# Performance work log

Measured on AMD Instinct MI355X. Metric: run time of the kernel, lower is better.

The kernel has to match this reference:

```python
import jax, jax.numpy as jnp
import numpy as np

B, S, D = 8, 1024, 512


def setup_inputs() -> dict:
    key = jax.random.key(0)
    k1, k2, k3, k4, k5, k6, k7 = jax.random.split(key, 7)
    inp = jax.random.normal(k1, (B, S, D), dtype=jnp.float32)
    aspect = jax.random.normal(k2, (B, S, D), dtype=jnp.float32)
    # lengths in [S//2, S], with max exactly S (the module requires max(len)==S)
    inp_len = jax.random.randint(k3, (B,), S // 2, S + 1).astype(jnp.float32)
    inp_len = inp_len.at[0].set(float(S))
    lim = float(np.sqrt(6.0 / (D + D)))  # xavier_uniform bound
    w1 = jax.random.uniform(k4, (D, D), jnp.float32, -lim, lim)
    b1 = jax.random.uniform(k5, (D,), jnp.float32, -lim, lim)
    w2 = jax.random.uniform(k6, (D, D), jnp.float32, -lim, lim)
    b2 = jax.random.uniform(k7, (D,), jnp.float32, -lim, lim)
    return {"inp": inp, "inp_len": inp_len, "aspect": aspect,
            "w1": w1, "b1": b1, "w2": w2, "b2": b2}


def reference(inp, inp_len, aspect, w1, b1, w2, b2):
    # inp, aspect: [B,S,D]; inp_len: [B] float lengths with max == S
    Bv, Sv, Dv = inp.shape
    scale = jnp.sqrt(inp_len)[:, None, None]                      # [B,1,1]
    att = jnp.einsum('bsd,btd->bst', aspect, inp) / scale          # [B,S,S]
    # mask over the query (row) dimension, as in the original expand
    mask = (jnp.arange(Sv)[None, :] < inp_len.astype(jnp.int32)[:, None]).astype(inp.dtype)  # [B,S]
    exp = att * mask[:, :, None]
    att_n = exp / (jnp.sum(exp, axis=-1, keepdims=True) + 1e-4)    # linear (non-exp) normalize
    weighted = jnp.einsum('bst,btd->bsd', att_n, inp)              # [B,S,D]
    ffn_inp = weighted + (inp + aspect) * mask[:, :, None]
    # FFN: two square linears with relu, plus inner residual
    o1 = jax.nn.relu(jnp.einsum('bsd,ed->bse', ffn_inp, w1) + b1)
    o2 = jax.nn.relu(jnp.einsum('bsd,ed->bse', o1, w2) + b2)
    ffn_out = o2 + ffn_inp
    final = ffn_inp + ffn_out
    return final / jnp.linalg.norm(final, axis=2, keepdims=True)
```

## Files before the change

kernel.cpp:

```cpp
#include <hip/hip_runtime.h>

#define Bq 8
#define Sq 1024
#define Dq 512

typedef __attribute__((ext_vector_type(8))) short bf16x8;
typedef __attribute__((ext_vector_type(4))) float f32x4;

__device__ __forceinline__ unsigned short f2bf(float f) {
  unsigned int u = __float_as_uint(f);
  return (unsigned short)((u + 0x7fffu + ((u >> 16) & 1u)) >> 16);
}

__device__ __forceinline__ void load_lds16(const unsigned short* g, unsigned short* l) {
  __builtin_amdgcn_global_load_lds(
      (const __attribute__((address_space(1))) unsigned int*)g,
      (__attribute__((address_space(3))) unsigned int*)l, 16, 0, 0);
}


__global__ __launch_bounds__(256) void prep_t(
    const float* __restrict__ inp,
    unsigned short* __restrict__ inpT, float* __restrict__ partial) {
  __shared__ unsigned short tile[64][66];
  __shared__ float csum[16][64];
  int idx = blockIdx.x;
  int tid = threadIdx.x;
  int b = idx & 7, tt = (idx >> 3) & 15, dd = idx >> 7;
  int r = tid >> 4, c4 = (tid & 15) * 4;
  const float* src = inp + ((size_t)b * Sq + tt * 64) * Dq + dd * 64;
  float cp0 = 0.f, cp1 = 0.f, cp2 = 0.f, cp3 = 0.f;
#pragma unroll
  for (int p = 0; p < 4; ++p) {
    float4 v = *(const float4*)(src + (size_t)(r + p * 16) * Dq + c4);
    ushort4 o; o.x = f2bf(v.x); o.y = f2bf(v.y); o.z = f2bf(v.z); o.w = f2bf(v.w);
    *(ushort4*)&tile[r + p * 16][c4] = o;
    cp0 += v.x; cp1 += v.y; cp2 += v.z; cp3 += v.w;
  }
  csum[r][c4] = cp0; csum[r][c4 + 1] = cp1; csum[r][c4 + 2] = cp2; csum[r][c4 + 3] = cp3;
  __syncthreads();
  unsigned short* dst = inpT + (size_t)b * Dq * Sq + (size_t)dd * 64 * Sq + tt * 64;
#pragma unroll
  for (int p = 0; p < 4; ++p) {
    int d = (tid >> 4) + p * 16;
    int tq = (tid & 15) * 4;
    ushort4 o;
    o.x = tile[tq][d]; o.y = tile[tq + 1][d]; o.z = tile[tq + 2][d]; o.w = tile[tq + 3][d];
    *(ushort4*)(dst + (size_t)d * Sq + tq) = o;
  }
  if (tid < 64) {
    float s = 0.f;
#pragma unroll
    for (int rr = 0; rr < 16; ++rr) s += csum[rr][tid];
    partial[((size_t)b * 16 + tt) * Dq + dd * 64 + tid] = s;
  }
}

__global__ __launch_bounds__(512, 2) void gram_fac(
    const unsigned short* __restrict__ inpT, const float* __restrict__ partial,
    const float* __restrict__ aspect, const float* __restrict__ lenv,
    const float* __restrict__ w1, const float* __restrict__ w2,
    unsigned short* __restrict__ Gm, float* __restrict__ fac,
    unsigned short* __restrict__ asp_bf,
    unsigned short* __restrict__ w1b, unsigned short* __restrict__ w2b) {
  __shared__ unsigned short sA[2][64 * 64];
  __shared__ unsigned short sB[2][128 * 64];
  int idx = blockIdx.x;
  int tid = threadIdx.x;
  int lane = tid & 63, wave = tid >> 6;

  if (idx >= 672) {
    int blk = idx - 672;
    const float* src = (blk < 128) ? w1 : w2;
    unsigned short* dst = (blk < 128) ? w1b : w2b;
    int li = ((blk & 127) * 512 + tid) * 4;
    int n = li >> 9, k = li & 511;
    float4 v = *(const float4*)(src + li);
    ushort4 o; o.x = f2bf(v.x); o.y = f2bf(v.y); o.z = f2bf(v.z); o.w = f2bf(v.w);
    int x = ((k >> 3) & 3) ^ ((n >> 1) & 3);
    int off = (k >> 5) * 16384 + n * 32 + x * 8 + (k & 7);
    *(ushort4*)(dst + off) = o;
    return;
  }
  if (idx >= 416) {
    int blk = idx - 416;
    const float* s = aspect + (size_t)blk * 16384 + tid * 4;
    unsigned short* d = asp_bf + (size_t)blk * 16384 + tid * 4;
#pragma unroll
    for (int j = 0; j < 8; ++j) {
      float4 v = *(const float4*)(s + j * 2048);
      ushort4 o; o.x = f2bf(v.x); o.y = f2bf(v.y); o.z = f2bf(v.z); o.w = f2bf(v.w);
      *(ushort4*)(d + j * 2048) = o;
    }
    return;
  }
  if (idx >= 160) {
    float* cs = (float*)sA;
    int fblk = idx - 160;
    int b = fblk >> 5;
    int s0 = (fblk & 31) * 32;
    {
      int d = tid;
      float s = 0.f;
      const float* p = partial + (size_t)b * 16 * Dq + d;
#pragma unroll
      for (int t = 0; t < 16; ++t) s += p[t * Dq];
      cs[d] = s;
    }
    __syncthreads();
    int g = lane >> 4, lr = lane & 15;
    int row = s0 + wave * 4 + g;
    const float* a = aspect + ((size_t)b * Sq + row) * Dq + lr * 32;
    float sum = 0.f;
#pragma unroll
    for (int j = 0; j < 8; ++j) {
      float4 v = *(const float4*)(a + j * 4);
      const float* c = cs + lr * 32 + j * 4;
      sum += v.x * c[0] + v.y * c[1] + v.z * c[2] + v.w * c[3];
    }
#pragma unroll
    for (int off = 1; off < 16; off <<= 1) sum += __shfl_xor(sum, off, 64);
    if (lr == 0) {
      float len = lenv[b];
      float scale = sqrtf(len);
      float f = 0.f;
      if (row < (int)len) f = 1.f / (scale * (sum / scale + 1e-4f));
      fac[b * Sq + row] = f;
    }
    return;
  }

  static const signed char TI[20] = {0,0,0,0, 1,1,1,1, 2,2,2, 3,3,3, 4,4, 5,5, 6, 7};
  static const signed char TJ[20] = {0,1,2,3, 0,1,2,3, 1,2,3, 1,2,3, 2,3, 2,3, 3, 3};
  const int K = 1024;
  int b = idx & 7;
  int t = idx >> 3;
  int bm = TI[t], bn = TJ[t];
  const unsigned short* Ab = inpT + (size_t)b * Dq * Sq + (size_t)bm * 64 * K;
  const unsigned short* Bb = inpT + (size_t)b * Dq * Sq + (size_t)bn * 128 * K;
  int lr = lane & 15, lq = lane >> 4;
  int x7 = lr & 7;
  int t8 = tid >> 3, t7 = tid & 7;

  const unsigned short* gA = Ab + (size_t)t8 * K + (t7 ^ (t8 & 7)) * 8;
  const unsigned short* gB = Bb + (size_t)t8 * K + (t7 ^ (t8 & 7)) * 8;
  const unsigned short* gB2 = Bb + (size_t)(t8 + 64) * K + (t7 ^ (t8 & 7)) * 8;
  int dbase = tid * 8;

  f32x4 acc[2][2] = {};

  auto issue = [&](int buf, int k0) {
    load_lds16(gA + k0, &sA[buf][dbase]);
    load_lds16(gB + k0, &sB[buf][dbase]);
    load_lds16(gB2 + k0, &sB[buf][4096 + dbase]);
  };

  int wm = (wave & 1) * 32, wn = (wave >> 1) * 32;
  issue(0, 0);
#pragma unroll
  for (int it = 0; it < 16; ++it) {
    int cur = it & 1;
    if (it + 1 < 16) {
      issue(cur ^ 1, (it + 1) << 6);
      asm volatile("s_waitcnt vmcnt(3)" ::: "memory");
    } else {
      asm volatile("s_waitcnt vmcnt(0)" ::: "memory");
    }
    __builtin_amdgcn_s_barrier();
#pragma unroll
    for (int c = 0; c < 2; ++c) {
      int g = (c * 4 + lq) ^ x7;
      bf16x8 a0 = *(const bf16x8*)&sA[cur][((wm + lr) * 8 + g) * 8];
      bf16x8 a1 = *(const bf16x8*)&sA[cur][((wm + 16 + lr) * 8 + g) * 8];
      bf16x8 b0 = *(const bf16x8*)&sB[cur][((wn + lr) * 8 + g) * 8];
      bf16x8 b1 = *(const bf16x8*)&sB[cur][((wn + 16 + lr) * 8 + g) * 8];
      acc[0][0] = __builtin_amdgcn_mfma_f32_16x16x32_bf16(a0, b0, acc[0][0], 0, 0, 0);
      acc[0][1] = __builtin_amdgcn_mfma_f32_16x16x32_bf16(a0, b1, acc[0][1], 0, 0, 0);
      acc[1][0] = __builtin_amdgcn_mfma_f32_16x16x32_bf16(a1, b0, acc[1][0], 0, 0, 0);
      acc[1][1] = __builtin_amdgcn_mfma_f32_16x16x32_bf16(a1, b1, acc[1][1], 0, 0, 0);
    }
    asm volatile("s_waitcnt lgkmcnt(0)" ::: "memory");
    __builtin_amdgcn_sched_barrier(0);
    __builtin_amdgcn_s_barrier();
  }

  unsigned short* sP = sB[0];
  int kcl = wm >> 5;
#pragma unroll
  for (int mi = 0; mi < 2; ++mi)
#pragma unroll
    for (int ni = 0; ni < 2; ++ni)
#pragma unroll
      for (int i = 0; i < 4; ++i) {
        int rl = mi * 16 + lq * 4 + i;
        int nl = wn + ni * 16 + lr;
        int x = (rl >> 3) ^ ((nl >> 1) & 3);
        sP[kcl * 4096 + nl * 32 + x * 8 + (rl & 7)] = f2bf(acc[mi][ni][i]);
      }
  __syncthreads();
  unsigned short* Ob = Gm + (size_t)b * 512 * 512 + (size_t)(bm * 2) * 16384 +
                       (size_t)bn * 4096;
#pragma unroll
  for (int h = 0; h < 2; ++h)
    *(bf16x8*)(Ob + h * 16384 + tid * 8) = *(const bf16x8*)(sP + h * 4096 + tid * 8);
  __syncthreads();

#pragma unroll
  for (int mi = 0; mi < 2; ++mi)
#pragma unroll
    for (int ni = 0; ni < 2; ++ni)
#pragma unroll
      for (int i = 0; i < 4; ++i) {
        int rl = mi * 16 + lq * 4 + i;
        int nl = wn + ni * 16 + lr;
        int np = wm + rl;
        int x2 = ((nl & 31) >> 3) ^ ((np >> 1) & 3);
        sP[(nl >> 5) * 2048 + np * 32 + x2 * 8 + (nl & 7)] = f2bf(acc[mi][ni][i]);
      }
  __syncthreads();
  unsigned short* Ot = Gm + (size_t)b * 512 * 512 + (size_t)(bn * 4) * 16384 +
                       (size_t)bm * 2048;
#pragma unroll
  for (int h2 = 0; h2 < 2; ++h2) {
    int slot = h2 * 512 + tid;
    int ch = slot >> 8, wi = slot & 255;
    *(bf16x8*)(Ot + ch * 16384 + wi * 8) = *(const bf16x8*)(sP + ch * 2048 + wi * 8);
  }
}

#define MEGA_SMEM (32768 + 3 * 32768 + 1024)

__global__ __launch_bounds__(512, 1) void mega_ffn(
    const unsigned short* __restrict__ aspb, const unsigned short* __restrict__ G,
    const unsigned short* __restrict__ w1b, const unsigned short* __restrict__ w2b,
    const float* __restrict__ b1, const float* __restrict__ b2,
    const float* __restrict__ inp, const float* __restrict__ aspect,
    const float* __restrict__ fac, const float* __restrict__ lenv,
    float* __restrict__ out) {
  extern __shared__ char smem[];
  unsigned short* ldsA = (unsigned short*)smem;
  unsigned short* wbuf = (unsigned short*)(smem + 32768);
  float* ssqW = (float*)(smem + 32768 + 3 * 65536 / 2);
  int tid = threadIdx.x;
  int lane = tid & 63, wave = tid >> 6;
  int lr = lane & 15, lq = lane >> 4;
  int batch = blockIdx.x & 7;
  int pos = blockIdx.x >> 3;
  int r0 = batch * 1024 + pos * 32;
  int c0 = wave * 64;

  f32x4 acc[2][4];
  float ffnv[2][4][4];

  auto aoff = [&](int rr, int c) {
    int cq = c >> 3;
    return rr * 512 + ((cq ^ (rr & 7)) << 3) + (c & 7);
  };
  int bx = (lq ^ ((lr >> 1) & 3)) * 8;
  int rdbase = (c0 + lr) * 32 + bx;

  auto stage = [&](int buf, int kc, const unsigned short* Bp) {
    const unsigned short* src = Bp + kc * 16384 + wave * 2048 + lane * 8;
    unsigned short* dst = wbuf + buf * 16384 + wave * 2048 + lane * 8;
#pragma unroll
    for (int i = 0; i < 4; ++i) load_lds16(src + i * 512, dst + i * 512);
  };

  auto gemmPhase = [&](const unsigned short* Bp) {
#pragma unroll
    for (int m = 0; m < 2; ++m)
#pragma unroll
      for (int t = 0; t < 4; ++t) acc[m][t] = (f32x4){0.f, 0.f, 0.f, 0.f};
    stage(0, 0, Bp);
    stage(1, 1, Bp);
#pragma unroll
    for (int kc = 0; kc < 16; ++kc) {
      int cur = kc % 3;
      if (kc + 2 < 16) stage((kc + 2) % 3, kc + 2, Bp);
      if (kc < 14) {
        asm volatile("s_waitcnt vmcnt(8)" ::: "memory");
      } else if (kc == 14) {
        asm volatile("s_waitcnt vmcnt(4)" ::: "memory");
      } else {
        asm volatile("s_waitcnt vmcnt(0)" ::: "memory");
      }
      bf16x8 a0 = *(const bf16x8*)&ldsA[aoff(lr, kc * 32 + lq * 8)];
      bf16x8 a1 = *(const bf16x8*)&ldsA[aoff(16 + lr, kc * 32 + lq * 8)];
      bf16x8 bfr[4];
#pragma unroll
      for (int t = 0; t < 4; ++t)
        bfr[t] = *(const bf16x8*)&wbuf[cur * 16384 + rdbase + t * 512];
      __builtin_amdgcn_s_setprio(1);
#pragma unroll
      for (int t = 0; t < 4; ++t) {
        acc[0][t] = __builtin_amdgcn_mfma_f32_16x16x32_bf16(a0, bfr[t], acc[0][t], 0, 0, 0);
        acc[1][t] = __builtin_amdgcn_mfma_f32_16x16x32_bf16(a1, bfr[t], acc[1][t], 0, 0, 0);
      }
      __builtin_amdgcn_s_setprio(0);
    }
  };

#pragma unroll
  for (int h = 0; h < 8; ++h) {
    int s = h * 512 + tid;
    int rr = s >> 6, sq = s & 63;
    int cq = sq ^ (rr & 7);
    load_lds16(aspb + (size_t)(r0 + rr) * 512 + cq * 8, ldsA + s * 8);
  }
  asm volatile("s_waitcnt vmcnt(0)" ::: "memory");
  __syncthreads();

  gemmPhase(G + (size_t)batch * 512 * 512);
  int len = (int)lenv[batch];
  float facv[2][4];
#pragma unroll
  for (int m = 0; m < 2; ++m)
#pragma unroll
    for (int i = 0; i < 4; ++i) facv[m][i] = fac[r0 + m * 16 + lq * 4 + i];
  __syncthreads();
#pragma unroll
  for (int m = 0; m < 2; ++m)
#pragma unroll
    for (int t = 0; t < 4; ++t)
#pragma unroll
      for (int i = 0; i < 4; ++i) {
        int rr = m * 16 + lq * 4 + i;
        int gr = r0 + rr;
        size_t idx = (size_t)gr * 512 + c0 + t * 16 + lr;
        float add = ((gr & 1023) < len) ? (inp[idx] + aspect[idx]) : 0.f;
        float v = acc[m][t][i] * facv[m][i] + add;
        ffnv[m][t][i] = v;
        ldsA[aoff(rr, c0 + t * 16 + lr)] = f2bf(v);
      }
  __syncthreads();

  gemmPhase(w1b);
  float biasv[4];
#pragma unroll
  for (int t = 0; t < 4; ++t) biasv[t] = b1[c0 + t * 16 + lr];
  __syncthreads();
#pragma unroll
  for (int m = 0; m < 2; ++m)
#pragma unroll
    for (int t = 0; t < 4; ++t)
#pragma unroll
      for (int i = 0; i < 4; ++i) {
        int rr = m * 16 + lq * 4 + i;
        ldsA[aoff(rr, c0 + t * 16 + lr)] = f2bf(fmaxf(acc[m][t][i] + biasv[t], 0.f));
      }
  __syncthreads();

  gemmPhase(w2b);
#pragma unroll
  for (int t = 0; t < 4; ++t) biasv[t] = b2[c0 + t * 16 + lr];
  float ssq[2][4] = {{0.f, 0.f, 0.f, 0.f}, {0.f, 0.f, 0.f, 0.f}};
#pragma unroll
  for (int m = 0; m < 2; ++m)
#pragma unroll
    for (int t = 0; t < 4; ++t)
#pragma unroll
      for (int i = 0; i < 4; ++i) {
        float v = 2.f * ffnv[m][t][i] + fmaxf(acc[m][t][i] + biasv[t], 0.f);
        ffnv[m][t][i] = v;
        ssq[m][i] += v * v;
      }
#pragma unroll
  for (int off = 1; off < 16; off <<= 1)
#pragma unroll
    for (int m = 0; m < 2; ++m)
#pragma unroll
      for (int i = 0; i < 4; ++i) ssq[m][i] += __shfl_xor(ssq[m][i], off, 64);
  if (lr == 0)
#pragma unroll
    for (int m = 0; m < 2; ++m)
#pragma unroll
      for (int i = 0; i < 4; ++i) ssqW[wave * 32 + m * 16 + lq * 4 + i] = ssq[m][i];
  __syncthreads();
  float rn[2][4];
#pragma unroll
  for (int m = 0; m < 2; ++m)
#pragma unroll
    for (int i = 0; i < 4; ++i) {
      float s = 0.f;
#pragma unroll
      for (int w = 0; w < 8; ++w) s += ssqW[w * 32 + m * 16 + lq * 4 + i];
      rn[m][i] = 1.f / sqrtf(s);
    }
#pragma unroll
  for (int m = 0; m < 2; ++m)
#pragma unroll
    for (int t = 0; t < 4; ++t)
#pragma unroll
      for (int i = 0; i < 4; ++i) {
        int gr = r0 + m * 16 + lq * 4 + i;
        out[(size_t)gr * 512 + c0 + t * 16 + lr] = ffnv[m][t][i] * rn[m][i];
      }
}

extern "C" void kernel_launch(void* const* d_in, const int* in_sizes, int n_in,
                              void* d_out, int out_size, void* d_ws, size_t ws_size,
                              hipStream_t stream) {
  const float* inp = (const float*)d_in[0];
  const float* inp_len = (const float*)d_in[1];
  const float* aspect = (const float*)d_in[2];
  const float* w1 = (const float*)d_in[3];
  const float* b1 = (const float*)d_in[4];
  const float* w2 = (const float*)d_in[5];
  const float* b2 = (const float*)d_in[6];
  float* out = (float*)d_out;

  char* W = (char*)d_ws;
  const size_t MB = 1ull << 20;
  unsigned short* asp_bf = (unsigned short*)(W + 0);
  unsigned short* inpT   = (unsigned short*)(W + 8 * MB);
  unsigned short* Gm     = (unsigned short*)(W + 16 * MB);
  unsigned short* w1bf   = (unsigned short*)(W + 20 * MB);
  unsigned short* w2bf   = (unsigned short*)(W + 20 * MB + 512 * 1024);
  float*          partial= (float*)(W + 21 * MB);
  float*          fac    = (float*)(W + 22 * MB);

  prep_t<<<1024, 256, 0, stream>>>(inp, inpT, partial);

  gram_fac<<<928, 512, 0, stream>>>(inpT, partial, aspect, inp_len, w1, w2,
                                    Gm, fac, asp_bf, w1bf, w2bf);

  hipFuncSetAttribute((const void*)mega_ffn,
                      hipFuncAttributeMaxDynamicSharedMemorySize, MEGA_SMEM);
  mega_ffn<<<256, 512, MEGA_SMEM, stream>>>(
      asp_bf, Gm, w1bf, w2bf, b1, b2, inp, aspect, fac, inp_len, out);
}
```

Baseline: 133.5 us.

## Move casts into the prep kernel and fuse the fac computation into mega_ffn

The aspect and weight bf16 conversions move from the gram kernel into the first prep kernel, which becomes a 2048-block multi-role kernel. The gram kernel now only computes the Gram matrix. The per-row normalisation factor is computed inside mega_ffn from the column partial sums and kept in LDS, which removes the fac global buffer and its round trip. The aspect-tile LDS prefetch is cut to the 32 rows actually used, since wbuf is now borrowed as scratch. The trade-off: the gram kernel loses the independent work that overlapped with it, and mega_ffn gains extra aspect reads and a reduction before its first GEMM.

Result: slower. 138.2 us (+3.6%).

```diff
diff --git a/kernel.cpp b/kernel.cpp
--- a/kernel.cpp
+++ b/kernel.cpp
@@ -19,116 +19,76 @@
 }
 
 
-__global__ __launch_bounds__(256) void prep_t(
-    const float* __restrict__ inp,
-    unsigned short* __restrict__ inpT, float* __restrict__ partial) {
+__global__ __launch_bounds__(256) void prep_all(
+    const float* __restrict__ inp, const float* __restrict__ aspect,
+    const float* __restrict__ w1, const float* __restrict__ w2,
+    unsigned short* __restrict__ inpT, float* __restrict__ partial,
+    unsigned short* __restrict__ asp_bf,
+    unsigned short* __restrict__ w1b, unsigned short* __restrict__ w2b) {
   __shared__ unsigned short tile[64][66];
   __shared__ float csum[16][64];
   int idx = blockIdx.x;
   int tid = threadIdx.x;
-  int b = idx & 7, tt = (idx >> 3) & 15, dd = idx >> 7;
-  int r = tid >> 4, c4 = (tid & 15) * 4;
-  const float* src = inp + ((size_t)b * Sq + tt * 64) * Dq + dd * 64;
-  float cp0 = 0.f, cp1 = 0.f, cp2 = 0.f, cp3 = 0.f;
-#pragma unroll
-  for (int p = 0; p < 4; ++p) {
-    float4 v = *(const float4*)(src + (size_t)(r + p * 16) * Dq + c4);
-    ushort4 o; o.x = f2bf(v.x); o.y = f2bf(v.y); o.z = f2bf(v.z); o.w = f2bf(v.w);
-    *(ushort4*)&tile[r + p * 16][c4] = o;
-    cp0 += v.x; cp1 += v.y; cp2 += v.z; cp3 += v.w;
-  }
-  csum[r][c4] = cp0; csum[r][c4 + 1] = cp1; csum[r][c4 + 2] = cp2; csum[r][c4 + 3] = cp3;
-  __syncthreads();
-  unsigned short* dst = inpT + (size_t)b * Dq * Sq + (size_t)dd * 64 * Sq + tt * 64;
-#pragma unroll
-  for (int p = 0; p < 4; ++p) {
-    int d = (tid >> 4) + p * 16;
-    int tq = (tid & 15) * 4;
-    ushort4 o;
-    o.x = tile[tq][d]; o.y = tile[tq + 1][d]; o.z = tile[tq + 2][d]; o.w = tile[tq + 3][d];
-    *(ushort4*)(dst + (size_t)d * Sq + tq) = o;
-  }
-  if (tid < 64) {
-    float s = 0.f;
-#pragma unroll
-    for (int rr = 0; rr < 16; ++rr) s += csum[rr][tid];
-    partial[((size_t)b * 16 + tt) * Dq + dd * 64 + tid] = s;
-  }
-}
-
-__global__ __launch_bounds__(512, 2) void gram_fac(
-    const unsigned short* __restrict__ inpT, const float* __restrict__ partial,
-    const float* __restrict__ aspect, const float* __restrict__ lenv,
-    const float* __restrict__ w1, const float* __restrict__ w2,
-    unsigned short* __restrict__ Gm, float* __restrict__ fac,
-    unsigned short* __restrict__ asp_bf,
-    unsigned short* __restrict__ w1b, unsigned short* __restrict__ w2b) {
-  __shared__ unsigned short sA[2][64 * 64];
-  __shared__ unsigned short sB[2][128 * 64];
-  int idx = blockIdx.x;
-  int tid = threadIdx.x;
-  int lane = tid & 63, wave = tid >> 6;
-
-  if (idx >= 672) {
-    int blk = idx - 672;
-    const float* src = (blk < 128) ? w1 : w2;
-    unsigned short* dst = (blk < 128) ? w1b : w2b;
-    int li = ((blk & 127) * 512 + tid) * 4;
+  if (idx < 1024) {
+    int b = idx & 7, tt = (idx >> 3) & 15, dd = idx >> 7;
+    int r = tid >> 4, c4 = (tid & 15) * 4;
+    const float* src = inp + ((size_t)b * Sq + tt * 64) * Dq + dd * 64;
+    float cp0 = 0.f, cp1 = 0.f, cp2 = 0.f, cp3 = 0.f;
+#pragma unroll
+    for (int p = 0; p < 4; ++p) {
+      float4 v = *(const float4*)(src + (size_t)(r + p * 16) * Dq + c4);
+      ushort4 o; o.x = f2bf(v.x); o.y = f2bf(v.y); o.z = f2bf(v.z); o.w = f2bf(v.w);
+      *(ushort4*)&tile[r + p * 16][c4] = o;
+      cp0 += v.x; cp1 += v.y; cp2 += v.z; cp3 += v.w;
+    }
+    csum[r][c4] = cp0; csum[r][c4 + 1] = cp1; csum[r][c4 + 2] = cp2; csum[r][c4 + 3] = cp3;
+    __syncthreads();
+    unsigned short* dst = inpT + (size_t)b * Dq * Sq + (size_t)dd * 64 * Sq + tt * 64;
+#pragma unroll
+    for (int p = 0; p < 4; ++p) {
+      int d = (tid >> 4) + p * 16;
+      int tq = (tid & 15) * 4;
+      ushort4 o;
+      o.x = tile[tq][d]; o.y = tile[tq + 1][d]; o.z = tile[tq + 2][d]; o.w = tile[tq + 3][d];
+      *(ushort4*)(dst + (size_t)d * Sq + tq) = o;
+    }
+    if (tid < 64) {
+      float s = 0.f;
+#pragma unroll
+      for (int rr = 0; rr < 16; ++rr) s += csum[rr][tid];
+      partial[((size_t)b * 16 + tt) * Dq + dd * 64 + tid] = s;
+    }
+  } else if (idx < 1536) {
+    int blk = idx - 1024;
+    const float* s = aspect + (size_t)blk * 8192 + tid * 4;
+    unsigned short* d = asp_bf + (size_t)blk * 8192 + tid * 4;
+#pragma unroll
+    for (int j = 0; j < 8; ++j) {
+      float4 v = *(const float4*)(s + j * 1024);
+      ushort4 o; o.x = f2bf(v.x); o.y = f2bf(v.y); o.z = f2bf(v.z); o.w = f2bf(v.w);
+      *(ushort4*)(d + j * 1024) = o;
+    }
+  } else {
+    int blk = idx - 1536;
+    const float* src = (blk < 256) ? w1 : w2;
+    unsigned short* dst = (blk < 256) ? w1b : w2b;
+    int li = ((blk & 255) * 256 + tid) * 4;
     int n = li >> 9, k = li & 511;
     float4 v = *(const float4*)(src + li);
     ushort4 o; o.x = f2bf(v.x); o.y = f2bf(v.y); o.z = f2bf(v.z); o.w = f2bf(v.w);
     int x = ((k >> 3) & 3) ^ ((n >> 1) & 3);
     int off = (k >> 5) * 16384 + n * 32 + x * 8 + (k & 7);
     *(ushort4*)(dst + off) = o;
-    return;
   }
-  if (idx >= 416) {
-    int blk = idx - 416;
-    const float* s = aspect + (size_t)blk * 16384 + tid * 4;
-    unsigned short* d = asp_bf + (size_t)blk * 16384 + tid * 4;
-#pragma unroll
-    for (int j = 0; j < 8; ++j) {
-      float4 v = *(const float4*)(s + j * 2048);
-      ushort4 o; o.x = f2bf(v.x); o.y = f2bf(v.y); o.z = f2bf(v.z); o.w = f2bf(v.w);
-      *(ushort4*)(d + j * 2048) = o;
-    }
-    return;
-  }
-  if (idx >= 160) {
-    float* cs = (float*)sA;
-    int fblk = idx - 160;
-    int b = fblk >> 5;
-    int s0 = (fblk & 31) * 32;
-    {
-      int d = tid;
-      float s = 0.f;
-      const float* p = partial + (size_t)b * 16 * Dq + d;
-#pragma unroll
-      for (int t = 0; t < 16; ++t) s += p[t * Dq];
-      cs[d] = s;
-    }
-    __syncthreads();
-    int g = lane >> 4, lr = lane & 15;
-    int row = s0 + wave * 4 + g;
-    const float* a = aspect + ((size_t)b * Sq + row) * Dq + lr * 32;
-    float sum = 0.f;
-#pragma unroll
-    for (int j = 0; j < 8; ++j) {
-      float4 v = *(const float4*)(a + j * 4);
-      const float* c = cs + lr * 32 + j * 4;
-      sum += v.x * c[0] + v.y * c[1] + v.z * c[2] + v.w * c[3];
-    }
-#pragma unroll
-    for (int off = 1; off < 16; off <<= 1) sum += __shfl_xor(sum, off, 64);
-    if (lr == 0) {
-      float len = lenv[b];
-      float scale = sqrtf(len);
-      float f = 0.f;
-      if (row < (int)len) f = 1.f / (scale * (sum / scale + 1e-4f));
-      fac[b * Sq + row] = f;
-    }
-    return;
-  }
+}
+
+__global__ __launch_bounds__(512, 2) void gram_only(
+    const unsigned short* __restrict__ inpT, unsigned short* __restrict__ Gm) {
+  __shared__ unsigned short sA[2][64 * 64];
+  __shared__ unsigned short sB[2][128 * 64];
+  int idx = blockIdx.x;
+  int tid = threadIdx.x;
+  int lane = tid & 63, wave = tid >> 6;
 
   static const signed char TI[20] = {0,0,0,0, 1,1,1,1, 2,2,2, 3,3,3, 4,4, 5,5, 6, 7};
   static const signed char TJ[20] = {0,1,2,3, 0,1,2,3, 1,2,3, 1,2,3, 2,3, 2,3, 3, 3};
@@ -228,19 +188,20 @@
   }
 }
 
-#define MEGA_SMEM (32768 + 3 * 32768 + 1024)
+#define MEGA_SMEM (32768 + 3 * 32768 + 1024 + 128)
 
 __global__ __launch_bounds__(512, 1) void mega_ffn(
     const unsigned short* __restrict__ aspb, const unsigned short* __restrict__ G,
     const unsigned short* __restrict__ w1b, const unsigned short* __restrict__ w2b,
     const float* __restrict__ b1, const float* __restrict__ b2,
     const float* __restrict__ inp, const float* __restrict__ aspect,
-    const float* __restrict__ fac, const float* __restrict__ lenv,
+    const float* __restrict__ partial, const float* __restrict__ lenv,
     float* __restrict__ out) {
   extern __shared__ char smem[];
   unsigned short* ldsA = (unsigned short*)smem;
   unsigned short* wbuf = (unsigned short*)(smem + 32768);
-  float* ssqW = (float*)(smem + 32768 + 3 * 65536 / 2);
+  float* ssqW = (float*)(smem + 32768 + 3 * 32768);
+  float* facL = (float*)(smem + 32768 + 3 * 32768 + 1024);
   int tid = threadIdx.x;
   int lane = tid & 63, wave = tid >> 6;
   int lr = lane & 15, lq = lane >> 4;
@@ -301,12 +262,41 @@
   };
 
 #pragma unroll
-  for (int h = 0; h < 8; ++h) {
+  for (int h = 0; h < 4; ++h) {
     int s = h * 512 + tid;
     int rr = s >> 6, sq = s & 63;
     int cq = sq ^ (rr & 7);
     load_lds16(aspb + (size_t)(r0 + rr) * 512 + cq * 8, ldsA + s * 8);
   }
+
+  {
+    float* cs = (float*)wbuf;
+    float s = 0.f;
+    const float* p = partial + (size_t)batch * 16 * Dq + tid;
+#pragma unroll
+    for (int t = 0; t < 16; ++t) s += p[t * Dq];
+    cs[tid] = s;
+    __syncthreads();
+    int g = lane >> 4;
+    int row = pos * 32 + wave * 4 + g;
+    const float* a = aspect + ((size_t)batch * Sq + row) * Dq + lr * 32;
+    float sum = 0.f;
+#pragma unroll
+    for (int j = 0; j < 8; ++j) {
+      float4 v = *(const float4*)(a + j * 4);
+      const float* c = cs + lr * 32 + j * 4;
+      sum += v.x * c[0] + v.y * c[1] + v.z * c[2] + v.w * c[3];
+    }
+#pragma unroll
+    for (int off = 1; off < 16; off <<= 1) sum += __shfl_xor(sum, off, 64);
+    if (lr == 0) {
+      float len = lenv[batch];
+      float scale = sqrtf(len);
+      float f = 0.f;
+      if (row < (int)len) f = 1.f / (scale * (sum / scale + 1e-4f));
+      facL[wave * 4 + g] = f;
+    }
+  }
   asm volatile("s_waitcnt vmcnt(0)" ::: "memory");
   __syncthreads();
 
@@ -316,7 +306,7 @@
 #pragma unroll
   for (int m = 0; m < 2; ++m)
 #pragma unroll
-    for (int i = 0; i < 4; ++i) facv[m][i] = fac[r0 + m * 16 + lq * 4 + i];
+    for (int i = 0; i < 4; ++i) facv[m][i] = facL[m * 16 + lq * 4 + i];
   __syncthreads();
 #pragma unroll
   for (int m = 0; m < 2; ++m)
@@ -417,15 +407,14 @@
   unsigned short* w1bf   = (unsigned short*)(W + 20 * MB);
   unsigned short* w2bf   = (unsigned short*)(W + 20 * MB + 512 * 1024);
   float*          partial= (float*)(W + 21 * MB);
-  float*          fac    = (float*)(W + 22 * MB);
-
-  prep_t<<<1024, 256, 0, stream>>>(inp, inpT, partial);
-
-  gram_fac<<<928, 512, 0, stream>>>(inpT, partial, aspect, inp_len, w1, w2,
-                                    Gm, fac, asp_bf, w1bf, w2bf);
+
+  prep_all<<<2048, 256, 0, stream>>>(inp, aspect, w1, w2,
+                                     inpT, partial, asp_bf, w1bf, w2bf);
+
+  gram_only<<<160, 512, 0, stream>>>(inpT, Gm);
 
   hipFuncSetAttribute((const void*)mega_ffn,
                       hipFuncAttributeMaxDynamicSharedMemorySize, MEGA_SMEM);
   mega_ffn<<<256, 512, MEGA_SMEM, stream>>>(
-      asp_bf, Gm, w1bf, w2bf, b1, b2, inp, aspect, fac, inp_len, out);
-}
+      asp_bf, Gm, w1bf, w2bf, b1, b2, inp, aspect, partial, inp_len, out);
+}
```
